# Optimization experiments

Hardware: AMD Instinct MI355X
Metric: run time of the kernel (lower is better)

Reference implementation:

```python
import jax, jax.numpy as jnp
import numpy as np

NEG_BIG = -9e15
ALPHA = 0.2  # LeakyReLU negative slope


def setup_inputs() -> dict:
    key = jax.random.key(0)
    k1, k2, k3, k4 = jax.random.split(key, 4)
    N, Fin, Fout = 8192, 256, 256
    input_ = jax.random.normal(k1, (N, Fin), dtype=jnp.float32)
    adj = jax.random.randint(k2, (N, N), 0, 2, dtype=jnp.int32)
    # xavier_uniform with gain=1.414
    limW = 1.414 * np.sqrt(6.0 / (Fin + Fout))
    W = jax.random.uniform(k3, (Fin, Fout), minval=-limW, maxval=limW, dtype=jnp.float32)
    lima = 1.414 * np.sqrt(6.0 / (2 * Fout + 1))
    a = jax.random.uniform(k4, (2 * Fout, 1), minval=-lima, maxval=lima, dtype=jnp.float32)
    return {"input_": input_, "adj": adj, "W": W, "a": a}


def reference(input_, adj, W, a):
    # h: [N, F]
    h = input_ @ W
    F = h.shape[1]
    # Decompose cat([h_i, h_j]) @ a into per-node projections summed by broadcast
    src = h @ a[:F, 0]   # [N]  contribution of row node i
    dst = h @ a[F:, 0]   # [N]  contribution of col node j
    e = jax.nn.leaky_relu(src[:, None] + dst[None, :], negative_slope=ALPHA)  # [N, N]
    e = jnp.where(adj > 0, e, NEG_BIG)
    attention = jax.nn.softmax(e, axis=1)
    h_prime = attention @ h  # [N, F]
    return jax.nn.relu(h_prime)  # concat=True
```

## Files before the change

### kernel.cpp

```cpp
#include <hip/hip_runtime.h>
#include <math.h>

#define NN 8192
#define FF 256
#define ALPHA 0.2f
#define SS 8
#define JSEG (NN / SS)
#define STEPS (JSEG / 32)
#define BI 128

typedef __bf16 bf16x8 __attribute__((ext_vector_type(8)));
typedef __bf16 bf16x4 __attribute__((ext_vector_type(4)));
typedef float  f32x4  __attribute__((ext_vector_type(4)));

__device__ __forceinline__ void dma16(const void* g, void* l) {
    __builtin_amdgcn_global_load_lds((const __attribute__((address_space(1))) void*)g,
                                     (__attribute__((address_space(3))) void*)l,
                                     16, 0, 0);
}

#define VMCNT0   asm volatile("s_waitcnt vmcnt(0)" ::: "memory")
#define LGKM0    asm volatile("s_waitcnt lgkmcnt(0)" ::: "memory")
#define BARRIER  asm volatile("s_barrier" ::: "memory")
#define FENCE    asm volatile("" ::: "memory")

__global__ __launch_bounds__(256) void k0_wt(const float* __restrict__ W,
                                             __bf16* __restrict__ WT) {
    __shared__ float ts[64][65];
    const int t = threadIdx.x;
    const int k0 = blockIdx.x * 64;
    const int n0 = blockIdx.y * 64;
    #pragma unroll
    for (int r = 0; r < 4; ++r) {
        int krow = r * 16 + (t >> 4);
        int nc4 = (t & 15) * 4;
        *(float4*)&ts[krow][nc4] = *(const float4*)&W[(size_t)(k0 + krow) * FF + n0 + nc4];
    }
    __syncthreads();
    const int nloc = t >> 2;
    const int kc = (t & 3) * 16;
    union { bf16x8 v[2]; __bf16 e[16]; } hi, lo;
    #pragma unroll
    for (int u = 0; u < 16; ++u) {
        float x = ts[kc + u][nloc];
        __bf16 h1 = (__bf16)x;
        hi.e[u] = h1;
        lo.e[u] = (__bf16)(x - (float)h1);
    }
    size_t base = (size_t)(n0 + nloc) * FF + k0 + kc;
    *(bf16x8*)&WT[base] = hi.v[0];
    *(bf16x8*)&WT[base + 8] = hi.v[1];
    size_t lbase = (size_t)FF * FF + base;
    *(bf16x8*)&WT[lbase] = lo.v[0];
    *(bf16x8*)&WT[lbase + 8] = lo.v[1];
}

__global__ __launch_bounds__(256) void k1_h(const float* __restrict__ X,
                                            const __bf16* __restrict__ WT,
                                            const float* __restrict__ a,
                                            __bf16* __restrict__ hT,
                                            float* __restrict__ src,
                                            float* __restrict__ dst,
                                            unsigned* __restrict__ maxd) {
    __shared__ __bf16 ax[2][32][40];
    __shared__ float hs[32][264];
    __shared__ float red[2][4][32];
    const int t = threadIdx.x;
    const int i0 = blockIdx.x * 32;
    const int l = t & 63, wv = t >> 6, ln = l & 15, g = l >> 4;
    f32x4 acc[2][4];
    #pragma unroll
    for (int mt = 0; mt < 2; ++mt)
        #pragma unroll
        for (int nt = 0; nt < 4; ++nt)
            acc[mt][nt] = (f32x4){0.f, 0.f, 0.f, 0.f};

    for (int ks = 0; ks < 8; ++ks) {
        const int k0 = ks * 32;
        {
            int row = t >> 3, c4 = (t & 7) * 4;
            float4 xv = *(const float4*)&X[(size_t)(i0 + row) * FF + k0 + c4];
            bf16x4 hi4, lo4;
            float xs_[4] = {xv.x, xv.y, xv.z, xv.w};
            #pragma unroll
            for (int u = 0; u < 4; ++u) {
                __bf16 h1 = (__bf16)xs_[u];
                hi4[u] = h1;
                lo4[u] = (__bf16)(xs_[u] - (float)h1);
            }
            *(bf16x4*)&ax[0][row][c4] = hi4;
            *(bf16x4*)&ax[1][row][c4] = lo4;
        }
        __syncthreads();
        bf16x8 ah[2], al[2];
        ah[0] = *(bf16x8*)&ax[0][ln][g * 8];
        ah[1] = *(bf16x8*)&ax[0][16 + ln][g * 8];
        al[0] = *(bf16x8*)&ax[1][ln][g * 8];
        al[1] = *(bf16x8*)&ax[1][16 + ln][g * 8];
        #pragma unroll
        for (int nt = 0; nt < 4; ++nt) {
            const int n = wv * 64 + nt * 16 + ln;
            bf16x8 bh8 = *(const bf16x8*)&WT[(size_t)n * FF + k0 + g * 8];
            bf16x8 bl8 = *(const bf16x8*)&WT[(size_t)(FF + n) * FF + k0 + g * 8];
            #pragma unroll
            for (int mt = 0; mt < 2; ++mt) {
                acc[mt][nt] = __builtin_amdgcn_mfma_f32_16x16x32_bf16(ah[mt], bh8, acc[mt][nt], 0, 0, 0);
                acc[mt][nt] = __builtin_amdgcn_mfma_f32_16x16x32_bf16(ah[mt], bl8, acc[mt][nt], 0, 0, 0);
                acc[mt][nt] = __builtin_amdgcn_mfma_f32_16x16x32_bf16(al[mt], bh8, acc[mt][nt], 0, 0, 0);
            }
        }
        __syncthreads();
    }
    float an[4], ad[4];
    #pragma unroll
    for (int nt = 0; nt < 4; ++nt) {
        an[nt] = a[wv * 64 + nt * 16 + ln];
        ad[nt] = a[FF + wv * 64 + nt * 16 + ln];
    }
    float sp[2][4], dp[2][4];
    #pragma unroll
    for (int mt = 0; mt < 2; ++mt)
        #pragma unroll
        for (int rg = 0; rg < 4; ++rg) { sp[mt][rg] = 0.f; dp[mt][rg] = 0.f; }
    #pragma unroll
    for (int mt = 0; mt < 2; ++mt)
        #pragma unroll
        for (int nt = 0; nt < 4; ++nt)
            #pragma unroll
            for (int rg = 0; rg < 4; ++rg) {
                float v = acc[mt][nt][rg];
                hs[mt * 16 + g * 4 + rg][wv * 64 + nt * 16 + ln] = v;
                sp[mt][rg] += v * an[nt];
                dp[mt][rg] += v * ad[nt];
            }
    #pragma unroll
    for (int mk = 1; mk < 16; mk <<= 1)
        #pragma unroll
        for (int mt = 0; mt < 2; ++mt)
            #pragma unroll
            for (int rg = 0; rg < 4; ++rg) {
                sp[mt][rg] += __shfl_xor(sp[mt][rg], mk);
                dp[mt][rg] += __shfl_xor(dp[mt][rg], mk);
            }
    if (ln == 0) {
        #pragma unroll
        for (int mt = 0; mt < 2; ++mt)
            #pragma unroll
            for (int rg = 0; rg < 4; ++rg) {
                red[0][wv][mt * 16 + g * 4 + rg] = sp[mt][rg];
                red[1][wv][mt * 16 + g * 4 + rg] = dp[mt][rg];
            }
    }
    __syncthreads();
    if (t < 32) {
        src[i0 + t] = red[0][0][t] + red[0][1][t] + red[0][2][t] + red[0][3][t];
        float dv_ = red[1][0][t] + red[1][1][t] + red[1][2][t] + red[1][3][t];
        dst[i0 + t] = dv_;
        unsigned u = __float_as_uint(dv_);
        unsigned key = (u & 0x80000000u) ? ~u : (u | 0x80000000u);
        atomicMax(maxd, key);
    }
    {
        const int f = t;
        const int seg_i = i0 >> 10;
        const int ilb = i0 & (JSEG - 1);
        #pragma unroll
        for (int jc = 0; jc < 4; ++jc) {
            union { bf16x8 v; __bf16 e[8]; } hi;
            #pragma unroll
            for (int u = 0; u < 8; ++u) {
                float x = hs[jc * 8 + u][f];
                hi.e[u] = (__bf16)x;
            }
            *(bf16x8*)&hT[((size_t)seg_i * FF + f) * JSEG + ilb + jc * 8] = hi.v;
        }
    }
}

__global__ __launch_bounds__(256) void k2a_pack(const int* __restrict__ adj,
                                                unsigned* __restrict__ bits,
                                                unsigned* __restrict__ maxd) {
    if (blockIdx.x == 0 && threadIdx.x == 0) maxd[0] = 0u;
    const size_t total4 = (size_t)NN * NN / 4;
    const int l = threadIdx.x & 63;
    const int base = l & 56;
    size_t t = (size_t)blockIdx.x * 256 + threadIdx.x;
    const size_t stride = (size_t)gridDim.x * 256;
    for (; t < total4; t += stride) {
        int4 v = ((const int4*)adj)[t];
        unsigned nib = (unsigned)(v.x > 0) | ((unsigned)(v.y > 0) << 1)
                     | ((unsigned)(v.z > 0) << 2) | ((unsigned)(v.w > 0) << 3);
        unsigned w = 0;
        #pragma unroll
        for (int k = 0; k < 8; ++k)
            w |= (unsigned)__shfl((int)nib, base + k) << (4 * k);
        if ((l & 7) == 0)
            bits[t >> 3] = w;
    }
}

__global__ __launch_bounds__(512, 4) void k3_attn(const unsigned* __restrict__ bits,
                                                  const __bf16* __restrict__ hT,
                                                  const float* __restrict__ src,
                                                  const float* __restrict__ dst,
                                                  const unsigned* __restrict__ maxd,
                                                  float* __restrict__ num,
                                                  float* __restrict__ den) {
    __shared__ __bf16 bh[2][1024 * 8];
    __shared__ float dsts[JSEG];
    const int t = threadIdx.x;
    const int l = t & 63, wv = t >> 6, ln = l & 15, g = l >> 4;
    const int seg = blockIdx.x & 7;
    const int it = blockIdx.x >> 3;
    const int i0 = it * BI;
    const int jbeg = seg * JSEG;
    const int row = i0 + wv * 16 + ln;
    const unsigned mk_ = maxd[0];
    const float maxdv = (mk_ & 0x80000000u) ? __uint_as_float(mk_ & 0x7fffffffu)
                                            : __uint_as_float(~mk_);
    const float src_r = src[row];
    const float e0 = src_r + maxdv;
    const float m_r = e0 > 0.f ? e0 : ALPHA * e0;

    const __bf16* hTs = hT + (size_t)seg * FF * JSEG;

    int ga[2], cb[2];
    #pragma unroll
    for (int r = 0; r < 2; ++r) {
        int cbase = r * 512 + wv * 64;
        int c = cbase + l;
        int f = c >> 2;
        int pc = c & 3;
        int jc = pc ^ ((f >> 1) & 3);
        ga[r] = f * JSEG + jc * 8;
        cb[r] = __builtin_amdgcn_readfirstlane(cbase);
    }
    const int rb = ln * 64 + ((g ^ ((ln >> 1) & 3)) * 16);
    const char* bh0 = (const char*)&bh[0][0] + rb;
    const char* bh1 = (const char*)&bh[1][0] + rb;

    const unsigned* grow = bits + (size_t)row * (NN / 32) + (jbeg >> 5);

    #pragma unroll
    for (int r = 0; r < 2; ++r)
        dma16(&hTs[ga[r]], &bh[0][cb[r] * 8]);
    FENCE;
    if (t < 256) *(float4*)&dsts[t * 4] = *(const float4*)&dst[jbeg + t * 4];
    uint2 wp = *(const uint2*)&grow[0];
    uint2 wpn = wp;
    __syncthreads();

    float den_reg = 0.f;
    f32x4 acc[16];
    #pragma unroll
    for (int nt = 0; nt < 16; ++nt) acc[nt] = (f32x4){0.f, 0.f, 0.f, 0.f};

#define K3_WCOMP(S_, MW_, AF_)                                                \
    {                                                                         \
        unsigned mb = ((MW_) >> (g * 8)) & 0xffu;                             \
        const float* dp_ = &dsts[(S_) * 32 + g * 8];                          \
        float4 dq0 = *(const float4*)dp_;                                     \
        float4 dq1 = *(const float4*)(dp_ + 4);                               \
        const float dv[8] = {dq0.x, dq0.y, dq0.z, dq0.w,                      \
                             dq1.x, dq1.y, dq1.z, dq1.w};                     \
        _Pragma("unroll")                                                     \
        for (int u = 0; u < 8; ++u) {                                         \
            float e = src_r + dv[u];                                          \
            e = e > 0.f ? e : ALPHA * e;                                      \
            float ex = __expf(e - m_r);                                       \
            float w = (mb & (1u << u)) ? ex : 0.f;                            \
            den_reg += w;                                                     \
            AF_.e[u] = (__bf16)w;                                             \
        }                                                                     \
    }

#define K3_MFMA(AF_, BP_)                                                     \
    {                                                                         \
        _Pragma("unroll")                                                     \
        for (int nt = 0; nt < 16; ++nt) {                                     \
            bf16x8 bfr = *(const bf16x8*)((BP_) + nt * 1024);                 \
            acc[nt] = __builtin_amdgcn_mfma_f32_16x16x32_bf16(                \
                AF_.v, bfr, acc[nt], 0, 0, 0);                                \
        }                                                                     \
    }

    for (int s = 0; s < STEPS; s += 2) {
        union { bf16x8 v; __bf16 e[8]; } afe;
        K3_WCOMP(s, wp.x, afe);
        FENCE; VMCNT0; LGKM0; BARRIER;
        #pragma unroll
        for (int r = 0; r < 2; ++r)
            dma16(&hTs[ga[r] + (s + 1) * 32], &bh[1][cb[r] * 8]);
        if (s + 2 < STEPS) wpn = *(const uint2*)&grow[s + 2];
        FENCE;
        K3_MFMA(afe, bh0);
        union { bf16x8 v; __bf16 e[8]; } afo;
        K3_WCOMP(s + 1, wp.y, afo);
        FENCE; VMCNT0; LGKM0; BARRIER;
        {
            int sn = (s + 2 < STEPS) ? s + 2 : 0;
            #pragma unroll
            for (int r = 0; r < 2; ++r)
                dma16(&hTs[ga[r] + sn * 32], &bh[0][cb[r] * 8]);
        }
        FENCE;
        K3_MFMA(afo, bh1);
        wp = wpn;
    }
    den_reg += __shfl_xor(den_reg, 16);
    den_reg += __shfl_xor(den_reg, 32);
    if (g == 0) den[(size_t)seg * NN + row] = den_reg;
    #pragma unroll
    for (int nt = 0; nt < 16; ++nt)
        #pragma unroll
        for (int rg = 0; rg < 4; ++rg)
            num[((size_t)seg * NN + i0 + wv * 16 + g * 4 + rg) * FF
                + nt * 16 + ln] = acc[nt][rg];
}

__global__ __launch_bounds__(256) void k4_out(const float* __restrict__ num,
                                              const float* __restrict__ den,
                                              float* __restrict__ out) {
    size_t f4 = (size_t)blockIdx.x * 256 + threadIdx.x;
    int i = (int)(f4 >> 6);
    int c4 = (int)(f4 & 63) << 2;
    float4 s = make_float4(0.f, 0.f, 0.f, 0.f);
    float d = 0.f;
    #pragma unroll
    for (int sg = 0; sg < SS; ++sg) {
        float4 v = *(const float4*)&num[((size_t)sg * NN + i) * FF + c4];
        s.x += v.x; s.y += v.y; s.z += v.z; s.w += v.w;
        d += den[(size_t)sg * NN + i];
    }
    float inv = 1.f / d;
    float4 o;
    o.x = fmaxf(s.x * inv, 0.f);
    o.y = fmaxf(s.y * inv, 0.f);
    o.z = fmaxf(s.z * inv, 0.f);
    o.w = fmaxf(s.w * inv, 0.f);
    *(float4*)&out[(size_t)i * FF + c4] = o;
}

extern "C" void kernel_launch(void* const* d_in, const int* in_sizes, int n_in,
                              void* d_out, int out_size, void* d_ws, size_t ws_size,
                              hipStream_t stream) {
    const float* X  = (const float*)d_in[0];
    const int*  adj = (const int*)d_in[1];
    const float* W  = (const float*)d_in[2];
    const float* a  = (const float*)d_in[3];
    float* out = (float*)d_out;
    char* ws = (char*)d_ws;

    const size_t off_hT   = 0;
    const size_t off_wt   = off_hT + (size_t)FF * NN * 2;
    const size_t off_src  = off_wt + (size_t)2 * FF * FF * 2;
    const size_t off_dst  = off_src + (size_t)NN * 4;
    const size_t off_maxd = off_dst + (size_t)NN * 4;
    const size_t off_num  = off_maxd + 256;
    const size_t off_den  = off_num + (size_t)SS * NN * FF * 4;
    const size_t off_bits = off_den + (size_t)SS * NN * 4;

    __bf16* hT_ws = (__bf16*)(ws + off_hT);
    __bf16* wt_ws = (__bf16*)(ws + off_wt);
    float* src_ws = (float*)(ws + off_src);
    float* dst_ws = (float*)(ws + off_dst);
    unsigned* maxd = (unsigned*)(ws + off_maxd);
    float* num_ws = (float*)(ws + off_num);
    float* den_ws = (float*)(ws + off_den);
    unsigned* bits_ws = (unsigned*)(ws + off_bits);

    k2a_pack<<<2048, 256, 0, stream>>>(adj, bits_ws, maxd);
    k0_wt<<<dim3(FF / 64, FF / 64), 256, 0, stream>>>(W, wt_ws);
    k1_h<<<NN / 32, 256, 0, stream>>>(X, wt_ws, a, hT_ws, src_ws, dst_ws, maxd);
    k3_attn<<<(NN / BI) * SS, 512, 0, stream>>>(bits_ws, hT_ws, src_ws, dst_ws, maxd,
                                                num_ws, den_ws);
    k4_out<<<(NN * FF / 4) / 256, 256, 0, stream>>>(num_ws, den_ws, out);
}
```

Measured before the change: 446.4 us.

## Give each attention wave two row tiles and fuse weight-transpose into adjacency pack

```diff
diff --git a/kernel.cpp b/kernel.cpp
--- a/kernel.cpp
+++ b/kernel.cpp
@@ -24,35 +24,58 @@
 #define BARRIER  asm volatile("s_barrier" ::: "memory")
 #define FENCE    asm volatile("" ::: "memory")
 
-__global__ __launch_bounds__(256) void k0_wt(const float* __restrict__ W,
-                                             __bf16* __restrict__ WT) {
+__global__ __launch_bounds__(256) void k02a(const float* __restrict__ W,
+                                            __bf16* __restrict__ WT,
+                                            const int* __restrict__ adj,
+                                            unsigned* __restrict__ bits,
+                                            unsigned* __restrict__ maxd) {
     __shared__ float ts[64][65];
     const int t = threadIdx.x;
-    const int k0 = blockIdx.x * 64;
-    const int n0 = blockIdx.y * 64;
-    #pragma unroll
-    for (int r = 0; r < 4; ++r) {
-        int krow = r * 16 + (t >> 4);
-        int nc4 = (t & 15) * 4;
-        *(float4*)&ts[krow][nc4] = *(const float4*)&W[(size_t)(k0 + krow) * FF + n0 + nc4];
-    }
-    __syncthreads();
-    const int nloc = t >> 2;
-    const int kc = (t & 3) * 16;
-    union { bf16x8 v[2]; __bf16 e[16]; } hi, lo;
-    #pragma unroll
-    for (int u = 0; u < 16; ++u) {
-        float x = ts[kc + u][nloc];
-        __bf16 h1 = (__bf16)x;
-        hi.e[u] = h1;
-        lo.e[u] = (__bf16)(x - (float)h1);
-    }
-    size_t base = (size_t)(n0 + nloc) * FF + k0 + kc;
-    *(bf16x8*)&WT[base] = hi.v[0];
-    *(bf16x8*)&WT[base + 8] = hi.v[1];
-    size_t lbase = (size_t)FF * FF + base;
-    *(bf16x8*)&WT[lbase] = lo.v[0];
-    *(bf16x8*)&WT[lbase + 8] = lo.v[1];
+    if (blockIdx.x < 16) {
+        const int k0 = (blockIdx.x & 3) * 64;
+        const int n0 = (blockIdx.x >> 2) * 64;
+        #pragma unroll
+        for (int r = 0; r < 4; ++r) {
+            int krow = r * 16 + (t >> 4);
+            int nc4 = (t & 15) * 4;
+            *(float4*)&ts[krow][nc4] = *(const float4*)&W[(size_t)(k0 + krow) * FF + n0 + nc4];
+        }
+        __syncthreads();
+        const int nloc = t >> 2;
+        const int kc = (t & 3) * 16;
+        union { bf16x8 v[2]; __bf16 e[16]; } hi, lo;
+        #pragma unroll
+        for (int u = 0; u < 16; ++u) {
+            float x = ts[kc + u][nloc];
+            __bf16 h1 = (__bf16)x;
+            hi.e[u] = h1;
+            lo.e[u] = (__bf16)(x - (float)h1);
+        }
+        size_t base = (size_t)(n0 + nloc) * FF + k0 + kc;
+        *(bf16x8*)&WT[base] = hi.v[0];
+        *(bf16x8*)&WT[base + 8] = hi.v[1];
+        size_t lbase = (size_t)FF * FF + base;
+        *(bf16x8*)&WT[lbase] = lo.v[0];
+        *(bf16x8*)&WT[lbase + 8] = lo.v[1];
+        return;
+    }
+    if (blockIdx.x == 16 && t == 0) maxd[0] = 0u;
+    const size_t total4 = (size_t)NN * NN / 4;
+    const int l = t & 63;
+    const int base = l & 56;
+    size_t p = (size_t)(blockIdx.x - 16) * 256 + t;
+    const size_t stride = (size_t)(gridDim.x - 16) * 256;
+    for (; p < total4; p += stride) {
+        int4 v = ((const int4*)adj)[p];
+        unsigned nib = (unsigned)(v.x > 0) | ((unsigned)(v.y > 0) << 1)
+                     | ((unsigned)(v.z > 0) << 2) | ((unsigned)(v.w > 0) << 3);
+        unsigned w = 0;
+        #pragma unroll
+        for (int k = 0; k < 8; ++k)
+            w |= (unsigned)__shfl((int)nib, base + k) << (4 * k);
+        if ((l & 7) == 0)
+            bits[p >> 3] = w;
+    }
 }
 
 __global__ __launch_bounds__(256) void k1_h(const float* __restrict__ X,
@@ -177,29 +200,7 @@
     }
 }
 
-__global__ __launch_bounds__(256) void k2a_pack(const int* __restrict__ adj,
-                                                unsigned* __restrict__ bits,
-                                                unsigned* __restrict__ maxd) {
-    if (blockIdx.x == 0 && threadIdx.x == 0) maxd[0] = 0u;
-    const size_t total4 = (size_t)NN * NN / 4;
-    const int l = threadIdx.x & 63;
-    const int base = l & 56;
-    size_t t = (size_t)blockIdx.x * 256 + threadIdx.x;
-    const size_t stride = (size_t)gridDim.x * 256;
-    for (; t < total4; t += stride) {
-        int4 v = ((const int4*)adj)[t];
-        unsigned nib = (unsigned)(v.x > 0) | ((unsigned)(v.y > 0) << 1)
-                     | ((unsigned)(v.z > 0) << 2) | ((unsigned)(v.w > 0) << 3);
-        unsigned w = 0;
-        #pragma unroll
-        for (int k = 0; k < 8; ++k)
-            w |= (unsigned)__shfl((int)nib, base + k) << (4 * k);
-        if ((l & 7) == 0)
-            bits[t >> 3] = w;
-    }
-}
-
-__global__ __launch_bounds__(512, 4) void k3_attn(const unsigned* __restrict__ bits,
+__global__ __launch_bounds__(256, 2) void k3_attn(const unsigned* __restrict__ bits,
                                                   const __bf16* __restrict__ hT,
                                                   const float* __restrict__ src,
                                                   const float* __restrict__ dst,
@@ -214,20 +215,24 @@
     const int it = blockIdx.x >> 3;
     const int i0 = it * BI;
     const int jbeg = seg * JSEG;
-    const int row = i0 + wv * 16 + ln;
+    const int row0 = i0 + wv * 32 + ln;
+    const int row1 = row0 + 16;
     const unsigned mk_ = maxd[0];
     const float maxdv = (mk_ & 0x80000000u) ? __uint_as_float(mk_ & 0x7fffffffu)
                                             : __uint_as_float(~mk_);
-    const float src_r = src[row];
-    const float e0 = src_r + maxdv;
-    const float m_r = e0 > 0.f ? e0 : ALPHA * e0;
+    const float s0 = src[row0];
+    const float s1 = src[row1];
+    const float e00 = s0 + maxdv;
+    const float m0 = e00 > 0.f ? e00 : ALPHA * e00;
+    const float e01 = s1 + maxdv;
+    const float m1 = e01 > 0.f ? e01 : ALPHA * e01;
 
     const __bf16* hTs = hT + (size_t)seg * FF * JSEG;
 
-    int ga[2], cb[2];
-    #pragma unroll
-    for (int r = 0; r < 2; ++r) {
-        int cbase = r * 512 + wv * 64;
+    int ga[4], cb[4];
+    #pragma unroll
+    for (int r = 0; r < 4; ++r) {
+        int cbase = r * 256 + wv * 64;
         int c = cbase + l;
         int f = c >> 2;
         int pc = c & 3;
@@ -239,25 +244,31 @@
     const char* bh0 = (const char*)&bh[0][0] + rb;
     const char* bh1 = (const char*)&bh[1][0] + rb;
 
-    const unsigned* grow = bits + (size_t)row * (NN / 32) + (jbeg >> 5);
-
-    #pragma unroll
-    for (int r = 0; r < 2; ++r)
+    const unsigned* grow0 = bits + (size_t)row0 * (NN / 32) + (jbeg >> 5);
+    const unsigned* grow1 = bits + (size_t)row1 * (NN / 32) + (jbeg >> 5);
+
+    #pragma unroll
+    for (int r = 0; r < 4; ++r)
         dma16(&hTs[ga[r]], &bh[0][cb[r] * 8]);
     FENCE;
-    if (t < 256) *(float4*)&dsts[t * 4] = *(const float4*)&dst[jbeg + t * 4];
-    uint2 wp = *(const uint2*)&grow[0];
-    uint2 wpn = wp;
+    *(float4*)&dsts[t * 4] = *(const float4*)&dst[jbeg + t * 4];
+    uint2 wpa = *(const uint2*)&grow0[0];
+    uint2 wpb = *(const uint2*)&grow1[0];
+    uint2 wpan = wpa, wpbn = wpb;
     __syncthreads();
 
-    float den_reg = 0.f;
-    f32x4 acc[16];
-    #pragma unroll
-    for (int nt = 0; nt < 16; ++nt) acc[nt] = (f32x4){0.f, 0.f, 0.f, 0.f};
-
-#define K3_WCOMP(S_, MW_, AF_)                                                \
+    float den0 = 0.f, den1 = 0.f;
+    f32x4 acc0[16], acc1[16];
+    #pragma unroll
+    for (int nt = 0; nt < 16; ++nt) {
+        acc0[nt] = (f32x4){0.f, 0.f, 0.f, 0.f};
+        acc1[nt] = (f32x4){0.f, 0.f, 0.f, 0.f};
+    }
+
+#define K3_WCOMP2(S_, MA_, MB_, AF0_, AF1_)                                   \
     {                                                                         \
-        unsigned mb = ((MW_) >> (g * 8)) & 0xffu;                             \
+        unsigned mba = ((MA_) >> (g * 8)) & 0xffu;                            \
+        unsigned mbb = ((MB_) >> (g * 8)) & 0xffu;                            \
         const float* dp_ = &dsts[(S_) * 32 + g * 8];                          \
         float4 dq0 = *(const float4*)dp_;                                     \
         float4 dq1 = *(const float4*)(dp_ + 4);                               \
@@ -265,57 +276,75 @@
                              dq1.x, dq1.y, dq1.z, dq1.w};                     \
         _Pragma("unroll")                                                     \
         for (int u = 0; u < 8; ++u) {                                         \
-            float e = src_r + dv[u];                                          \
-            e = e > 0.f ? e : ALPHA * e;                                      \
-            float ex = __expf(e - m_r);                                       \
-            float w = (mb & (1u << u)) ? ex : 0.f;                            \
-            den_reg += w;                                                     \
-            AF_.e[u] = (__bf16)w;                                             \
+            float ea = s0 + dv[u];                                            \
+            ea = ea > 0.f ? ea : ALPHA * ea;                                  \
+            float wa = (mba & (1u << u)) ? __expf(ea - m0) : 0.f;             \
+            den0 += wa;                                                       \
+            AF0_.e[u] = (__bf16)wa;                                           \
+            float eb = s1 + dv[u];                                            \
+            eb = eb > 0.f ? eb : ALPHA * eb;                                  \
+            float wb = (mbb & (1u << u)) ? __expf(eb - m1) : 0.f;             \
+            den1 += wb;                                                       \
+            AF1_.e[u] = (__bf16)wb;                                           \
         }                                                                     \
     }
 
-#define K3_MFMA(AF_, BP_)                                                     \
+#define K3_MFMA2(AF0_, AF1_, BP_)                                             \
     {                                                                         \
         _Pragma("unroll")                                                     \
         for (int nt = 0; nt < 16; ++nt) {                                     \
             bf16x8 bfr = *(const bf16x8*)((BP_) + nt * 1024);                 \
-            acc[nt] = __builtin_amdgcn_mfma_f32_16x16x32_bf16(                \
-                AF_.v, bfr, acc[nt], 0, 0, 0);                                \
+            acc0[nt] = __builtin_amdgcn_mfma_f32_16x16x32_bf16(               \
+                AF0_.v, bfr, acc0[nt], 0, 0, 0);                              \
+            acc1[nt] = __builtin_amdgcn_mfma_f32_16x16x32_bf16(               \
+                AF1_.v, bfr, acc1[nt], 0, 0, 0);                              \
         }                                                                     \
     }
 
     for (int s = 0; s < STEPS; s += 2) {
-        union { bf16x8 v; __bf16 e[8]; } afe;
-        K3_WCOMP(s, wp.x, afe);
+        union { bf16x8 v; __bf16 e[8]; } af0e, af1e;
+        K3_WCOMP2(s, wpa.x, wpb.x, af0e, af1e);
         FENCE; VMCNT0; LGKM0; BARRIER;
         #pragma unroll
-        for (int r = 0; r < 2; ++r)
+        for (int r = 0; r < 4; ++r)
             dma16(&hTs[ga[r] + (s + 1) * 32], &bh[1][cb[r] * 8]);
-        if (s + 2 < STEPS) wpn = *(const uint2*)&grow[s + 2];
+        if (s + 2 < STEPS) {
+            wpan = *(const uint2*)&grow0[s + 2];
+            wpbn = *(const uint2*)&grow1[s + 2];
+        }
         FENCE;
-        K3_MFMA(afe, bh0);
-        union { bf16x8 v; __bf16 e[8]; } afo;
-        K3_WCOMP(s + 1, wp.y, afo);
+        K3_MFMA2(af0e, af1e, bh0);
+        union { bf16x8 v; __bf16 e[8]; } af0o, af1o;
+        K3_WCOMP2(s + 1, wpa.y, wpb.y, af0o, af1o);
         FENCE; VMCNT0; LGKM0; BARRIER;
         {
             int sn = (s + 2 < STEPS) ? s + 2 : 0;
             #pragma unroll
-            for (int r = 0; r < 2; ++r)
+            for (int r = 0; r < 4; ++r)
                 dma16(&hTs[ga[r] + sn * 32], &bh[0][cb[r] * 8]);
         }
         FENCE;
-        K3_MFMA(afo, bh1);
-        wp = wpn;
-    }
-    den_reg += __shfl_xor(den_reg, 16);
-    den_reg += __shfl_xor(den_reg, 32);
-    if (g == 0) den[(size_t)seg * NN + row] = den_reg;
+        K3_MFMA2(af0o, af1o, bh1);
+        wpa = wpan;
+        wpb = wpbn;
+    }
+    den0 += __shfl_xor(den0, 16);
+    den0 += __shfl_xor(den0, 32);
+    den1 += __shfl_xor(den1, 16);
+    den1 += __shfl_xor(den1, 32);
+    if (g == 0) {
+        den[(size_t)seg * NN + row0] = den0;
+        den[(size_t)seg * NN + row1] = den1;
+    }
     #pragma unroll
     for (int nt = 0; nt < 16; ++nt)
         #pragma unroll
-        for (int rg = 0; rg < 4; ++rg)
-            num[((size_t)seg * NN + i0 + wv * 16 + g * 4 + rg) * FF
-                + nt * 16 + ln] = acc[nt][rg];
+        for (int rg = 0; rg < 4; ++rg) {
+            num[((size_t)seg * NN + i0 + wv * 32 + g * 4 + rg) * FF
+                + nt * 16 + ln] = acc0[nt][rg];
+            num[((size_t)seg * NN + i0 + wv * 32 + 16 + g * 4 + rg) * FF
+                + nt * 16 + ln] = acc1[nt][rg];
+        }
 }
 
 __global__ __launch_bounds__(256) void k4_out(const float* __restrict__ num,
@@ -369,10 +398,9 @@
     float* den_ws = (float*)(ws + off_den);
     unsigned* bits_ws = (unsigned*)(ws + off_bits);
 
-    k2a_pack<<<2048, 256, 0, stream>>>(adj, bits_ws, maxd);
-    k0_wt<<<dim3(FF / 64, FF / 64), 256, 0, stream>>>(W, wt_ws);
+    k02a<<<2064, 256, 0, stream>>>(W, wt_ws, adj, bits_ws, maxd);
     k1_h<<<NN / 32, 256, 0, stream>>>(X, wt_ws, a, hT_ws, src_ws, dst_ws, maxd);
-    k3_attn<<<(NN / BI) * SS, 512, 0, stream>>>(bits_ws, hT_ws, src_ws, dst_ws, maxd,
+    k3_attn<<<(NN / BI) * SS, 256, 0, stream>>>(bits_ws, hT_ws, src_ws, dst_ws, maxd,
                                                 num_ws, den_ws);
     k4_out<<<(NN * FF / 4) / 256, 256, 0, stream>>>(num_ws, den_ws, out);
 }
```

Result: slower. 458.5 us (+2.7%).

## Triple-buffer hT tiles with vmcnt(2) and stage adjacency bits in LDS

Applied to the files above, without the earlier changes.

```diff
diff --git a/kernel.cpp b/kernel.cpp
--- a/kernel.cpp
+++ b/kernel.cpp
@@ -19,7 +19,7 @@
                                      16, 0, 0);
 }
 
-#define VMCNT0   asm volatile("s_waitcnt vmcnt(0)" ::: "memory")
+#define VMCNT2   asm volatile("s_waitcnt vmcnt(2)" ::: "memory")
 #define LGKM0    asm volatile("s_waitcnt lgkmcnt(0)" ::: "memory")
 #define BARRIER  asm volatile("s_barrier" ::: "memory")
 #define FENCE    asm volatile("" ::: "memory")
@@ -206,7 +206,8 @@
                                                   const unsigned* __restrict__ maxd,
                                                   float* __restrict__ num,
                                                   float* __restrict__ den) {
-    __shared__ __bf16 bh[2][1024 * 8];
+    __shared__ __bf16 bh[3][1024 * 8];
+    __shared__ unsigned mlds[BI * 33];
     __shared__ float dsts[JSEG];
     const int t = threadIdx.x;
     const int l = t & 63, wv = t >> 6, ln = l & 15, g = l >> 4;
@@ -214,7 +215,8 @@
     const int it = blockIdx.x >> 3;
     const int i0 = it * BI;
     const int jbeg = seg * JSEG;
-    const int row = i0 + wv * 16 + ln;
+    const int rl = wv * 16 + ln;
+    const int row = i0 + rl;
     const unsigned mk_ = maxd[0];
     const float maxdv = (mk_ & 0x80000000u) ? __uint_as_float(mk_ & 0x7fffffffu)
                                             : __uint_as_float(~mk_);
@@ -236,76 +238,70 @@
         cb[r] = __builtin_amdgcn_readfirstlane(cbase);
     }
     const int rb = ln * 64 + ((g ^ ((ln >> 1) & 3)) * 16);
-    const char* bh0 = (const char*)&bh[0][0] + rb;
-    const char* bh1 = (const char*)&bh[1][0] + rb;
-
-    const unsigned* grow = bits + (size_t)row * (NN / 32) + (jbeg >> 5);
 
     #pragma unroll
     for (int r = 0; r < 2; ++r)
         dma16(&hTs[ga[r]], &bh[0][cb[r] * 8]);
     FENCE;
+    {
+        int r = t >> 2;
+        int c = (t & 3) * 8;
+        const unsigned* gsrc = bits + (size_t)(i0 + r) * (NN / 32) + (jbeg >> 5) + c;
+        uint4 w0 = *(const uint4*)gsrc;
+        uint4 w1 = *(const uint4*)(gsrc + 4);
+        unsigned* ldst = &mlds[r * 33 + c];
+        ldst[0] = w0.x; ldst[1] = w0.y; ldst[2] = w0.z; ldst[3] = w0.w;
+        ldst[4] = w1.x; ldst[5] = w1.y; ldst[6] = w1.z; ldst[7] = w1.w;
+    }
     if (t < 256) *(float4*)&dsts[t * 4] = *(const float4*)&dst[jbeg + t * 4];
-    uint2 wp = *(const uint2*)&grow[0];
-    uint2 wpn = wp;
     __syncthreads();
+
+    #pragma unroll
+    for (int r = 0; r < 2; ++r)
+        dma16(&hTs[ga[r] + 32], &bh[1][cb[r] * 8]);
+    FENCE;
 
     float den_reg = 0.f;
     f32x4 acc[16];
     #pragma unroll
     for (int nt = 0; nt < 16; ++nt) acc[nt] = (f32x4){0.f, 0.f, 0.f, 0.f};
 
-#define K3_WCOMP(S_, MW_, AF_)                                                \
-    {                                                                         \
-        unsigned mb = ((MW_) >> (g * 8)) & 0xffu;                             \
-        const float* dp_ = &dsts[(S_) * 32 + g * 8];                          \
-        float4 dq0 = *(const float4*)dp_;                                     \
-        float4 dq1 = *(const float4*)(dp_ + 4);                               \
-        const float dv[8] = {dq0.x, dq0.y, dq0.z, dq0.w,                      \
-                             dq1.x, dq1.y, dq1.z, dq1.w};                     \
-        _Pragma("unroll")                                                     \
-        for (int u = 0; u < 8; ++u) {                                         \
-            float e = src_r + dv[u];                                          \
-            e = e > 0.f ? e : ALPHA * e;                                      \
-            float ex = __expf(e - m_r);                                       \
-            float w = (mb & (1u << u)) ? ex : 0.f;                            \
-            den_reg += w;                                                     \
-            AF_.e[u] = (__bf16)w;                                             \
-        }                                                                     \
-    }
-
-#define K3_MFMA(AF_, BP_)                                                     \
-    {                                                                         \
-        _Pragma("unroll")                                                     \
-        for (int nt = 0; nt < 16; ++nt) {                                     \
-            bf16x8 bfr = *(const bf16x8*)((BP_) + nt * 1024);                 \
-            acc[nt] = __builtin_amdgcn_mfma_f32_16x16x32_bf16(                \
-                AF_.v, bfr, acc[nt], 0, 0, 0);                                \
-        }                                                                     \
-    }
-
-    for (int s = 0; s < STEPS; s += 2) {
-        union { bf16x8 v; __bf16 e[8]; } afe;
-        K3_WCOMP(s, wp.x, afe);
-        FENCE; VMCNT0; LGKM0; BARRIER;
-        #pragma unroll
-        for (int r = 0; r < 2; ++r)
-            dma16(&hTs[ga[r] + (s + 1) * 32], &bh[1][cb[r] * 8]);
-        if (s + 2 < STEPS) wpn = *(const uint2*)&grow[s + 2];
+    int cur = 0;
+    for (int s = 0; s < STEPS; ++s) {
+        unsigned mb = (mlds[rl * 33 + s] >> (g * 8)) & 0xffu;
+        const float* dp_ = &dsts[s * 32 + g * 8];
+        float4 dq0 = *(const float4*)dp_;
+        float4 dq1 = *(const float4*)(dp_ + 4);
+        const float dv[8] = {dq0.x, dq0.y, dq0.z, dq0.w,
+                             dq1.x, dq1.y, dq1.z, dq1.w};
+        union { bf16x8 v; __bf16 e[8]; } af;
+        #pragma unroll
+        for (int u = 0; u < 8; ++u) {
+            float e = src_r + dv[u];
+            e = e > 0.f ? e : ALPHA * e;
+            float ex = __expf(e - m_r);
+            float w = (mb & (1u << u)) ? ex : 0.f;
+            den_reg += w;
+            af.e[u] = (__bf16)w;
+        }
+        FENCE; VMCNT2; LGKM0; BARRIER;
+        {
+            int sn = s + 2;
+            if (sn >= STEPS) sn -= STEPS;
+            int db = cur + 2;
+            if (db >= 3) db -= 3;
+            #pragma unroll
+            for (int r = 0; r < 2; ++r)
+                dma16(&hTs[ga[r] + sn * 32], &bh[db][cb[r] * 8]);
+        }
         FENCE;
-        K3_MFMA(afe, bh0);
-        union { bf16x8 v; __bf16 e[8]; } afo;
-        K3_WCOMP(s + 1, wp.y, afo);
-        FENCE; VMCNT0; LGKM0; BARRIER;
-        {
-            int sn = (s + 2 < STEPS) ? s + 2 : 0;
-            #pragma unroll
-            for (int r = 0; r < 2; ++r)
-                dma16(&hTs[ga[r] + sn * 32], &bh[0][cb[r] * 8]);
-        }
-        FENCE;
-        K3_MFMA(afo, bh1);
-        wp = wpn;
+        const char* bp = (const char*)&bh[0][0] + cur * 16384 + rb;
+        #pragma unroll
+        for (int nt = 0; nt < 16; ++nt) {
+            bf16x8 bfr = *(const bf16x8*)(bp + nt * 1024);
+            acc[nt] = __builtin_amdgcn_mfma_f32_16x16x32_bf16(af.v, bfr, acc[nt], 0, 0, 0);
+        }
+        if (++cur == 3) cur = 0;
     }
     den_reg += __shfl_xor(den_reg, 16);
     den_reg += __shfl_xor(den_reg, 32);
```

Result: no change. 447.9 us (+0.3%).
